# Kernel optimization log

Measured on AMD Instinct MI355X. Metric: run time of the kernel, lower is better.

The kernel has to match this reference:

```python
import jax, jax.numpy as jnp
import numpy as np

B, S, H = 2, 2048, 2048
NH, NKV, D = 16, 4, 128      # heads, kv heads, head_dim
GROUPS = NH // NKV
WIN = 1024                    # sliding window
EPS = 1e-5
THETA = 10000.0
NEG = -1e9


def _rms_norm(x, w):
    # over last dim (head_dim)
    var = jnp.mean(x * x, axis=-1, keepdims=True)
    return x * jax.lax.rsqrt(var + EPS) * w


def _rotate_half(x):
    x1, x2 = jnp.split(x, 2, axis=-1)
    return jnp.concatenate([-x2, x1], axis=-1)


def _apply_rope(q, k, cos, sin):
    # q: [B,NH,S,D], k: [B,NKV,S,D], cos/sin: [B,S,D]
    c = cos[:, None, :, :]
    s = sin[:, None, :, :]
    q = q * c + _rotate_half(q) * s
    k = k * c + _rotate_half(k) * s
    return q, k


def setup_inputs() -> dict:
    key = jax.random.key(0)
    ks = jax.random.split(key, 8)
    std = 0.02
    hidden_states = jax.random.normal(ks[0], (B, S, H), dtype=jnp.float32)
    Wq = jax.random.normal(ks[1], (NH * D, H), dtype=jnp.float32) * std
    Wk = jax.random.normal(ks[2], (NKV * D, H), dtype=jnp.float32) * std
    Wv = jax.random.normal(ks[3], (NKV * D, H), dtype=jnp.float32) * std
    Wo = jax.random.normal(ks[4], (H, NH * D), dtype=jnp.float32) * std
    Wg = jax.random.normal(ks[5], (NH * D, H), dtype=jnp.float32) * std
    q_norm_w = jnp.ones((D,), dtype=jnp.float32)
    k_norm_w = jnp.ones((D,), dtype=jnp.float32)
    # RoPE tables
    inv_freq = 1.0 / (THETA ** (jnp.arange(0, D, 2, dtype=jnp.float32) / D))
    pos = jnp.arange(S, dtype=jnp.float32)
    freqs = jnp.einsum('s,d->sd', pos, inv_freq)          # [S, D/2]
    emb = jnp.concatenate([freqs, freqs], axis=-1)        # [S, D]
    cos = jnp.broadcast_to(jnp.cos(emb)[None], (B, S, D)).astype(jnp.float32)
    sin = jnp.broadcast_to(jnp.sin(emb)[None], (B, S, D)).astype(jnp.float32)
    i = jnp.arange(S)[:, None]
    j = jnp.arange(S)[None, :]
    allowed = (j <= i) & (i - j < WIN)
    attention_mask = jnp.where(allowed, 0.0, NEG).astype(jnp.float32)[None, None]  # [1,1,S,S]
    return {
        'hidden_states': hidden_states, 'cos': cos, 'sin': sin,
        'attention_mask': attention_mask,
        'Wq': Wq, 'Wk': Wk, 'Wv': Wv, 'Wo': Wo, 'Wg': Wg,
        'q_norm_w': q_norm_w, 'k_norm_w': k_norm_w,
    }


def reference(hidden_states, cos, sin, attention_mask, Wq, Wk, Wv, Wo, Wg, q_norm_w, k_norm_w):
    x = hidden_states                                  # [B,S,H]
    q = (x @ Wq.T).reshape(B, S, NH, D)
    k = (x @ Wk.T).reshape(B, S, NKV, D)
    v = (x @ Wv.T).reshape(B, S, NKV, D)
    gate = x @ Wg.T                                    # [B,S,NH*D]
    q = _rms_norm(q, q_norm_w)
    k = _rms_norm(k, k_norm_w)
    q = q.transpose(0, 2, 1, 3)                        # [B,NH,S,D]
    k = k.transpose(0, 2, 1, 3)                        # [B,NKV,S,D]
    v = v.transpose(0, 2, 1, 3)
    # local (sliding) attention layer -> RoPE applied
    q, k = _apply_rope(q, k, cos, sin)
    # GQA: repeat kv heads
    k = jnp.repeat(k, GROUPS, axis=1)                  # [B,NH,S,D]
    v = jnp.repeat(v, GROUPS, axis=1)
    scaling = D ** -0.5
    scores = jnp.einsum('bhqd,bhkd->bhqk', q, k) * scaling
    scores = scores + attention_mask                   # broadcast [1,1,S,S]
    probs = jax.nn.softmax(scores.astype(jnp.float32), axis=-1).astype(q.dtype)
    out = jnp.einsum('bhqk,bhkd->bhqd', probs, v)      # [B,NH,S,D]
    out = out.transpose(0, 2, 1, 3).reshape(B, S, NH * D)
    out = out * jax.nn.sigmoid(gate)
    return out @ Wo.T                                  # [B,S,H]
```

## Files before the change

### kernel.cpp

```cpp
#include <hip/hip_runtime.h>
#include <hip/hip_bf16.h>

#define B_    2
#define S_    2048
#define H_    2048
#define NH_   16
#define NKV_  4
#define D_    128
#define WIN_  1024

typedef __attribute__((ext_vector_type(8))) short short8;
typedef __attribute__((ext_vector_type(4))) float f32x4;

__device__ __forceinline__ void gl2lds16(const void* g, void* l) {
  __builtin_amdgcn_global_load_lds(
      (const __attribute__((address_space(1))) void*)g,
      (__attribute__((address_space(3))) void*)l, 16, 0, 0);
}

__device__ __forceinline__ unsigned short f2bf(float x) {
  union { float f; unsigned int u; } v; v.f = x;
  unsigned int r = v.u + 0x7fffu + ((v.u >> 16) & 1u);
  return (unsigned short)(r >> 16);
}
__device__ __forceinline__ float bf2f(unsigned short u) {
  union { unsigned int i; float f; } v; v.i = ((unsigned int)u) << 16; return v.f;
}

#define CVT_TOTAL 5767168L
__global__ __launch_bounds__(256) void convert_all(
    const float* __restrict__ hs, const float* __restrict__ wq,
    const float* __restrict__ wk, const float* __restrict__ wv,
    const float* __restrict__ wg, const float* __restrict__ wo,
    unsigned short* __restrict__ xb, unsigned short* __restrict__ wall,
    unsigned short* __restrict__ wob) {
  long i = (long)blockIdx.x * 256 + threadIdx.x;
  if (i >= CVT_TOTAL) return;
  const float4* src; ushort4* dst;
  if (i < 2097152)      { src = (const float4*)hs + i;                         dst = (ushort4*)xb + i; }
  else if (i < 3145728) { long j = i - 2097152; src = (const float4*)wq + j;   dst = (ushort4*)wall + j; }
  else if (i < 3407872) { long j = i - 3145728; src = (const float4*)wk + j;   dst = (ushort4*)wall + 1048576 + j; }
  else if (i < 3670016) { long j = i - 3407872; src = (const float4*)wv + j;   dst = (ushort4*)wall + 1310720 + j; }
  else if (i < 4718592) { long j = i - 3670016; src = (const float4*)wg + j;   dst = (ushort4*)wall + 1572864 + j; }
  else                  { long j = i - 4718592; src = (const float4*)wo + j;   dst = (ushort4*)wob + j; }
  float4 v = *src;
  ushort4 o; o.x = f2bf(v.x); o.y = f2bf(v.y); o.z = f2bf(v.z); o.w = f2bf(v.w);
  *dst = o;
}

template <bool OUT_BF16>
__global__ __launch_bounds__(256) void gemm_bt(
    const unsigned short* __restrict__ A,
    const unsigned short* __restrict__ Bm,
    void* __restrict__ Cv, int M, int N, int K)
{
  __shared__ unsigned short As[128 * 64];
  __shared__ unsigned short Bs[128 * 64];
  const int t = threadIdx.x;
  const int lane = t & 63, wave = t >> 6;
  const int quad = lane >> 4, rl = lane & 15;
  const int bm = blockIdx.x * 128, bn = blockIdx.y * 128;
  const int wm = (wave >> 1) * 64, wn = (wave & 1) * 64;
  const int ldsbase = (t & ~63) * 8;

  f32x4 acc[4][4];
#pragma unroll
  for (int i = 0; i < 4; i++)
#pragma unroll
    for (int j = 0; j < 4; j++) acc[i][j] = (f32x4){0.f, 0.f, 0.f, 0.f};

  for (int k0 = 0; k0 < K; k0 += 64) {
#pragma unroll
    for (int i = 0; i < 4; i++) {
      int tt = i * 256 + t;
      int row = tt >> 3;
      int lc = (tt & 7) ^ (row & 7);
      gl2lds16(A + (long)(bm + row) * K + k0 + lc * 8, As + i * 2048 + ldsbase);
      gl2lds16(Bm + (long)(bn + row) * K + k0 + lc * 8, Bs + i * 2048 + ldsbase);
    }
    __syncthreads();
#pragma unroll
    for (int kk = 0; kk < 2; kk++) {
      short8 af[4], bfr[4];
#pragma unroll
      for (int i = 0; i < 4; i++) {
        int row = wm + i * 16 + rl;
        af[i] = *(const short8*)(As + row * 64 + (((kk * 4 + quad) ^ (row & 7)) * 8));
      }
#pragma unroll
      for (int j = 0; j < 4; j++) {
        int row = wn + j * 16 + rl;
        bfr[j] = *(const short8*)(Bs + row * 64 + (((kk * 4 + quad) ^ (row & 7)) * 8));
      }
#pragma unroll
      for (int i = 0; i < 4; i++)
#pragma unroll
        for (int j = 0; j < 4; j++)
          acc[i][j] = __builtin_amdgcn_mfma_f32_16x16x32_bf16(af[i], bfr[j], acc[i][j], 0, 0, 0);
    }
    __syncthreads();
  }
#pragma unroll
  for (int i = 0; i < 4; i++) {
    int row0 = bm + wm + i * 16 + quad * 4;
#pragma unroll
    for (int j = 0; j < 4; j++) {
      int col = bn + wn + j * 16 + rl;
#pragma unroll
      for (int r = 0; r < 4; r++) {
        if (OUT_BF16)
          ((unsigned short*)Cv)[(long)(row0 + r) * N + col] = f2bf(acc[i][j][r]);
        else
          ((float*)Cv)[(long)(row0 + r) * N + col] = acc[i][j][r];
      }
    }
  }
}

__global__ __launch_bounds__(256) void pack_and_transpose(
    const unsigned short* __restrict__ qkvg,
    const float* __restrict__ cosb, const float* __restrict__ sinb,
    const float* __restrict__ qw, const float* __restrict__ kw,
    unsigned short* __restrict__ qb, unsigned short* __restrict__ kb,
    unsigned short* __restrict__ vt)
{
  __shared__ unsigned short tile[64][136];
  int t = threadIdx.x;
  if (blockIdx.x >= 20480) {
    int blk = blockIdx.x - 20480;
    int st = blk & 31, kv = (blk >> 5) & 3, b = blk >> 7;
    int s0 = st * 64;
#pragma unroll
    for (int i = 0; i < 4; i++) {
      int idx = i * 256 + t;
      int r = idx >> 4, c = (idx & 15) * 8;
      short8 v = *(const short8*)(qkvg + (long)(b * S_ + s0 + r) * 5120 + 2560 + kv * 128 + c);
      *(short8*)(&tile[r][c]) = v;
    }
    __syncthreads();
    long vo = (long)(b * NKV_ + kv) * 128;
#pragma unroll
    for (int i = 0; i < 8; i++) {
      int idx = i * 256 + t;
      int d = idx >> 4, sc = idx & 15;
      ushort4 o;
      o.x = tile[sc * 4 + 0][d]; o.y = tile[sc * 4 + 1][d];
      o.z = tile[sc * 4 + 2][d]; o.w = tile[sc * 4 + 3][d];
      *(ushort4*)(vt + (vo + d) * S_ + s0 + sc * 4) = o;
    }
    return;
  }
  int lane = t & 63, wave = t >> 6;
  long gw = (long)blockIdx.x * 4 + wave;
  int hu = (int)(gw % 20);
  long bs = gw / 20;
  int b = (int)(bs / S_);
  int s = (int)(bs % S_);
  const unsigned short* row = qkvg + bs * 5120;

  bool isq = hu < 16;
  const unsigned short* base = isq ? (row + hu * 128) : (row + 2048 + (hu - 16) * 128);
  float x1 = bf2f(base[lane]), x2 = bf2f(base[lane + 64]);
  float ss = x1 * x1 + x2 * x2;
#pragma unroll
  for (int m = 1; m < 64; m <<= 1) ss += __shfl_xor(ss, m, 64);
  float inv = rsqrtf(ss * (1.0f / 128.0f) + 1e-5f);
  const float* w = isq ? qw : kw;
  float n1 = x1 * inv * w[lane], n2 = x2 * inv * w[lane + 64];
  const float* cp = cosb + bs * 128;
  const float* sp = sinb + bs * 128;
  float o1 = n1 * cp[lane] - n2 * sp[lane];
  float o2 = n2 * cp[lane + 64] + n1 * sp[lane + 64];
  if (isq) {
    long o = ((long)(b * NH_ + hu) * S_ + s) * 128;
    qb[o + lane] = f2bf(o1); qb[o + lane + 64] = f2bf(o2);
  } else {
    long o = ((long)(b * NKV_ + (hu - 16)) * S_ + s) * 128;
    kb[o + lane] = f2bf(o1); kb[o + lane + 64] = f2bf(o2);
  }
}

#define KSTR 136
#define VSTR 72
__global__ __launch_bounds__(256, 2) void attn_kernel(
    const unsigned short* __restrict__ qb,
    const unsigned short* __restrict__ kbuf,
    const unsigned short* __restrict__ vt,
    const unsigned short* __restrict__ qkvg,
    unsigned short* __restrict__ aout)
{
  __shared__ unsigned short Ks[64 * KSTR];
  __shared__ unsigned short Vs[128 * VSTR];
  __shared__ unsigned short Ps[4][2][16 * VSTR];
  int t = threadIdx.x, lane = t & 63, wave = t >> 6;
  int quad = lane >> 4, rl = lane & 15;
  int blk = blockIdx.x;
  int qh = blk & 1;
  int qt = 31 - ((blk >> 1) & 31);
  int kv = (blk >> 6) & 3, b = blk >> 8;
  int h = kv * 4 + wave;
  int q0 = qt * 64;

  const unsigned short* qhead = qb + (((long)(b * NH_ + h)) * S_) * 128;
  short8 qf[2][4];
#pragma unroll
  for (int mt = 0; mt < 2; mt++)
#pragma unroll
    for (int ks = 0; ks < 4; ks++)
      qf[mt][ks] = *(const short8*)(qhead +
          (long)(q0 + qh * 32 + mt * 16 + rl) * 128 + ks * 32 + quad * 8);

  f32x4 oacc[2][8];
#pragma unroll
  for (int mt = 0; mt < 2; mt++)
#pragma unroll
    for (int j = 0; j < 8; j++) oacc[mt][j] = (f32x4){0.f, 0.f, 0.f, 0.f};
  float m_r[2][4], l_r[2][4];
#pragma unroll
  for (int mt = 0; mt < 2; mt++)
#pragma unroll
    for (int r = 0; r < 4; r++) { m_r[mt][r] = -1e9f; l_r[mt][r] = 0.f; }

  const unsigned short* kbase_p = kbuf + ((long)(b * NKV_ + kv)) * S_ * 128;
  const unsigned short* vbase_p = vt + ((long)(b * NKV_ + kv)) * 128 * S_;
  int t_lo = qt - 16; if (t_lo < 0) t_lo = 0;

  int kr[4], kc[4], vr[4], vc[4];
#pragma unroll
  for (int i = 0; i < 4; i++) {
    int idx = i * 256 + t;
    kr[i] = idx >> 4; kc[i] = (idx & 15) * 8;
    vr[i] = idx >> 3; vc[i] = (idx & 7) * 8;
  }

  {
    int kb0 = t_lo * 64;
    short8 kv0[4], vv0[4];
#pragma unroll
    for (int i = 0; i < 4; i++) {
      kv0[i] = *(const short8*)(kbase_p + (long)(kb0 + kr[i]) * 128 + kc[i]);
      vv0[i] = *(const short8*)(vbase_p + (long)vr[i] * S_ + kb0 + vc[i]);
    }
#pragma unroll
    for (int i = 0; i < 4; i++) {
      *(short8*)(Ks + kr[i] * KSTR + kc[i]) = kv0[i];
      *(short8*)(Vs + vr[i] * VSTR + vc[i]) = vv0[i];
    }
  }
  __syncthreads();

  const float scale = 0.08838834764831845f;
  for (int kt = t_lo; kt <= qt; ++kt) {
    int kb0 = kt * 64;
    short8 kpre[4], vpre[4];
    if (kt < qt) {
      int nb0 = kb0 + 64;
#pragma unroll
      for (int i = 0; i < 4; i++) {
        kpre[i] = *(const short8*)(kbase_p + (long)(nb0 + kr[i]) * 128 + kc[i]);
        vpre[i] = *(const short8*)(vbase_p + (long)vr[i] * S_ + nb0 + vc[i]);
      }
    }

    f32x4 sc[2][4];
#pragma unroll
    for (int nt = 0; nt < 4; nt++) {
      f32x4 c0 = (f32x4){0.f, 0.f, 0.f, 0.f};
      f32x4 c1 = (f32x4){0.f, 0.f, 0.f, 0.f};
#pragma unroll
      for (int ks = 0; ks < 4; ks++) {
        short8 bfrag = *(const short8*)(Ks + (nt * 16 + rl) * KSTR + (ks * 4 + quad) * 8);
        c0 = __builtin_amdgcn_mfma_f32_16x16x32_bf16(qf[0][ks], bfrag, c0, 0, 0, 0);
        c1 = __builtin_amdgcn_mfma_f32_16x16x32_bf16(qf[1][ks], bfrag, c1, 0, 0, 0);
      }
      sc[0][nt] = c0; sc[1][nt] = c1;
    }
#pragma unroll
    for (int mt = 0; mt < 2; mt++) {
#pragma unroll
      for (int nt = 0; nt < 4; nt++)
#pragma unroll
        for (int r = 0; r < 4; r++) {
          int i_row = q0 + qh * 32 + mt * 16 + quad * 4 + r;
          int j_col = kb0 + nt * 16 + rl;
          bool ok = (j_col <= i_row) && (i_row - j_col < WIN_);
          sc[mt][nt][r] = ok ? sc[mt][nt][r] * scale : -1e9f;
        }
#pragma unroll
      for (int r = 0; r < 4; r++) {
        float mx = fmaxf(fmaxf(sc[mt][0][r], sc[mt][1][r]),
                         fmaxf(sc[mt][2][r], sc[mt][3][r]));
#pragma unroll
        for (int m = 1; m < 16; m <<= 1) mx = fmaxf(mx, __shfl_xor(mx, m, 64));
        float newm = fmaxf(m_r[mt][r], mx);
        float alpha = __expf(m_r[mt][r] - newm);
        float p0 = __expf(sc[mt][0][r] - newm), p1 = __expf(sc[mt][1][r] - newm);
        float p2 = __expf(sc[mt][2][r] - newm), p3 = __expf(sc[mt][3][r] - newm);
        float rs = p0 + p1 + p2 + p3;
#pragma unroll
        for (int m = 1; m < 16; m <<= 1) rs += __shfl_xor(rs, m, 64);
        l_r[mt][r] = l_r[mt][r] * alpha + rs;
        m_r[mt][r] = newm;
#pragma unroll
        for (int j = 0; j < 8; j++) oacc[mt][j][r] *= alpha;
        int prow = (quad * 4 + r) * VSTR;
        unsigned short* pw = &Ps[wave][mt][prow];
        pw[0 * 16 + rl] = f2bf(p0);
        pw[1 * 16 + rl] = f2bf(p1);
        pw[2 * 16 + rl] = f2bf(p2);
        pw[3 * 16 + rl] = f2bf(p3);
      }
    }
#pragma unroll
    for (int ks2 = 0; ks2 < 2; ks2++) {
      short8 af0 = *(const short8*)(&Ps[wave][0][rl * VSTR + (ks2 * 4 + quad) * 8]);
      short8 af1 = *(const short8*)(&Ps[wave][1][rl * VSTR + (ks2 * 4 + quad) * 8]);
#pragma unroll
      for (int j = 0; j < 8; j++) {
        short8 bf2 = *(const short8*)(Vs + (j * 16 + rl) * VSTR + (ks2 * 4 + quad) * 8);
        oacc[0][j] = __builtin_amdgcn_mfma_f32_16x16x32_bf16(af0, bf2, oacc[0][j], 0, 0, 0);
        oacc[1][j] = __builtin_amdgcn_mfma_f32_16x16x32_bf16(af1, bf2, oacc[1][j], 0, 0, 0);
      }
    }
    if (kt < qt) {
      __syncthreads();
#pragma unroll
      for (int i = 0; i < 4; i++) {
        *(short8*)(Ks + kr[i] * KSTR + kc[i]) = kpre[i];
        *(short8*)(Vs + vr[i] * VSTR + vc[i]) = vpre[i];
      }
      __syncthreads();
    }
  }

#pragma unroll
  for (int mt = 0; mt < 2; mt++)
#pragma unroll
    for (int r = 0; r < 4; r++) {
      int s_idx = q0 + qh * 32 + mt * 16 + quad * 4 + r;
      float invl = 1.0f / l_r[mt][r];
      long rowoff = (long)(b * S_ + s_idx);
      const unsigned short* grow = qkvg + rowoff * 5120 + 3072 + h * 128;
      unsigned short* orow = aout + rowoff * 2048 + h * 128;
#pragma unroll
      for (int j = 0; j < 8; j++) {
        int d = j * 16 + rl;
        float o = oacc[mt][j][r] * invl;
        float g = bf2f(grow[d]);
        o = o / (1.0f + __expf(-g));
        orow[d] = f2bf(o);
      }
    }
}

extern "C" void kernel_launch(void* const* d_in, const int* in_sizes, int n_in,
                              void* d_out, int out_size, void* d_ws, size_t ws_size,
                              hipStream_t stream) {
  (void)in_sizes; (void)n_in; (void)out_size; (void)ws_size;
  const float* hs   = (const float*)d_in[0];
  const float* cosb = (const float*)d_in[1];
  const float* sinb = (const float*)d_in[2];
  const float* Wq = (const float*)d_in[4];
  const float* Wk = (const float*)d_in[5];
  const float* Wv = (const float*)d_in[6];
  const float* Wo = (const float*)d_in[7];
  const float* Wg = (const float*)d_in[8];
  const float* qw = (const float*)d_in[9];
  const float* kw = (const float*)d_in[10];
  float* out = (float*)d_out;

  char* ws = (char*)d_ws;
  unsigned short* Xb   = (unsigned short*)ws; ws += (size_t)4096 * 2048 * 2;
  unsigned short* Wall = (unsigned short*)ws; ws += (size_t)5120 * 2048 * 2;
  unsigned short* Wob  = (unsigned short*)ws; ws += (size_t)2048 * 2048 * 2;
  unsigned short* qkvg = (unsigned short*)ws; ws += (size_t)4096 * 5120 * 2;
  unsigned short* qb   = (unsigned short*)ws; ws += (size_t)B_ * NH_ * S_ * D_ * 2;
  unsigned short* kbuf = (unsigned short*)ws; ws += (size_t)B_ * NKV_ * S_ * D_ * 2;
  unsigned short* vtb  = (unsigned short*)ws; ws += (size_t)B_ * NKV_ * S_ * D_ * 2;
  unsigned short* aout = (unsigned short*)ws; ws += (size_t)4096 * 2048 * 2;

  convert_all<<<(int)((CVT_TOTAL + 255) / 256), 256, 0, stream>>>(
      hs, Wq, Wk, Wv, Wg, Wo, Xb, Wall, Wob);
  gemm_bt<true><<<dim3(32, 40), 256, 0, stream>>>(Xb, Wall, (void*)qkvg, 4096, 5120, 2048);
  pack_and_transpose<<<20736, 256, 0, stream>>>(qkvg, cosb, sinb, qw, kw, qb, kbuf, vtb);
  attn_kernel<<<512, 256, 0, stream>>>(qb, kbuf, vtb, qkvg, aout);
  gemm_bt<false><<<dim3(32, 16), 256, 0, stream>>>(aout, Wob, (void*)out, 4096, 2048, 2048);
}
```

Baseline: 403.8 us.

## Split attention query tiles to 16 rows per wave, doubling grid and occupancy

Each wave now handles 16 query rows instead of 32, so the attention grid grows from 512 to 1024 blocks and launch bounds allow 3 blocks per CU. Block index decoding is reordered so blocks sharing a query tile sit next to each other, and the online-softmax rescale is skipped when no row max increases. MFMA sections are wrapped in s_setprio. The intent is more parallelism and less register pressure. The cost is that each K/V tile loaded into LDS is reused across fewer query rows, which adds global-to-LDS traffic.

After: 393.4 us. -2.6%, faster.

```diff
diff --git a/kernel.cpp b/kernel.cpp
--- a/kernel.cpp
+++ b/kernel.cpp
@@ -182,7 +182,8 @@
 
 #define KSTR 136
 #define VSTR 72
-__global__ __launch_bounds__(256, 2) void attn_kernel(
+#define PSTR 68
+__global__ __launch_bounds__(256, 3) void attn_kernel(
     const unsigned short* __restrict__ qb,
     const unsigned short* __restrict__ kbuf,
     const unsigned short* __restrict__ vt,
@@ -191,35 +192,29 @@
 {
   __shared__ unsigned short Ks[64 * KSTR];
   __shared__ unsigned short Vs[128 * VSTR];
-  __shared__ unsigned short Ps[4][2][16 * VSTR];
+  __shared__ unsigned short Ps[4][16 * PSTR];
   int t = threadIdx.x, lane = t & 63, wave = t >> 6;
   int quad = lane >> 4, rl = lane & 15;
   int blk = blockIdx.x;
-  int qh = blk & 1;
-  int qt = 31 - ((blk >> 1) & 31);
-  int kv = (blk >> 6) & 3, b = blk >> 8;
+  int qt = 31 - (blk >> 5);
+  int qu = blk & 3;
+  int kv = (blk >> 2) & 3;
+  int b  = (blk >> 4) & 1;
   int h = kv * 4 + wave;
-  int q0 = qt * 64;
+  int q0 = qt * 64 + qu * 16;
 
   const unsigned short* qhead = qb + (((long)(b * NH_ + h)) * S_) * 128;
-  short8 qf[2][4];
-#pragma unroll
-  for (int mt = 0; mt < 2; mt++)
-#pragma unroll
-    for (int ks = 0; ks < 4; ks++)
-      qf[mt][ks] = *(const short8*)(qhead +
-          (long)(q0 + qh * 32 + mt * 16 + rl) * 128 + ks * 32 + quad * 8);
-
-  f32x4 oacc[2][8];
-#pragma unroll
-  for (int mt = 0; mt < 2; mt++)
-#pragma unroll
-    for (int j = 0; j < 8; j++) oacc[mt][j] = (f32x4){0.f, 0.f, 0.f, 0.f};
-  float m_r[2][4], l_r[2][4];
-#pragma unroll
-  for (int mt = 0; mt < 2; mt++)
-#pragma unroll
-    for (int r = 0; r < 4; r++) { m_r[mt][r] = -1e9f; l_r[mt][r] = 0.f; }
+  short8 qf[4];
+#pragma unroll
+  for (int ks = 0; ks < 4; ks++)
+    qf[ks] = *(const short8*)(qhead + (long)(q0 + rl) * 128 + ks * 32 + quad * 8);
+
+  f32x4 oacc[8];
+#pragma unroll
+  for (int j = 0; j < 8; j++) oacc[j] = (f32x4){0.f, 0.f, 0.f, 0.f};
+  float m_r[4], l_r[4];
+#pragma unroll
+  for (int r = 0; r < 4; r++) { m_r[r] = -1e9f; l_r[r] = 0.f; }
 
   const unsigned short* kbase_p = kbuf + ((long)(b * NKV_ + kv)) * S_ * 128;
   const unsigned short* vbase_p = vt + ((long)(b * NKV_ + kv)) * 128 * S_;
@@ -262,66 +257,78 @@
       }
     }
 
-    f32x4 sc[2][4];
+    f32x4 sc[4];
+    __builtin_amdgcn_s_setprio(1);
 #pragma unroll
     for (int nt = 0; nt < 4; nt++) {
       f32x4 c0 = (f32x4){0.f, 0.f, 0.f, 0.f};
-      f32x4 c1 = (f32x4){0.f, 0.f, 0.f, 0.f};
 #pragma unroll
       for (int ks = 0; ks < 4; ks++) {
         short8 bfrag = *(const short8*)(Ks + (nt * 16 + rl) * KSTR + (ks * 4 + quad) * 8);
-        c0 = __builtin_amdgcn_mfma_f32_16x16x32_bf16(qf[0][ks], bfrag, c0, 0, 0, 0);
-        c1 = __builtin_amdgcn_mfma_f32_16x16x32_bf16(qf[1][ks], bfrag, c1, 0, 0, 0);
-      }
-      sc[0][nt] = c0; sc[1][nt] = c1;
-    }
-#pragma unroll
-    for (int mt = 0; mt < 2; mt++) {
-#pragma unroll
-      for (int nt = 0; nt < 4; nt++)
-#pragma unroll
-        for (int r = 0; r < 4; r++) {
-          int i_row = q0 + qh * 32 + mt * 16 + quad * 4 + r;
-          int j_col = kb0 + nt * 16 + rl;
-          bool ok = (j_col <= i_row) && (i_row - j_col < WIN_);
-          sc[mt][nt][r] = ok ? sc[mt][nt][r] * scale : -1e9f;
-        }
+        c0 = __builtin_amdgcn_mfma_f32_16x16x32_bf16(qf[ks], bfrag, c0, 0, 0, 0);
+      }
+      sc[nt] = c0;
+    }
+    __builtin_amdgcn_s_setprio(0);
+
+#pragma unroll
+    for (int nt = 0; nt < 4; nt++)
 #pragma unroll
       for (int r = 0; r < 4; r++) {
-        float mx = fmaxf(fmaxf(sc[mt][0][r], sc[mt][1][r]),
-                         fmaxf(sc[mt][2][r], sc[mt][3][r]));
-#pragma unroll
-        for (int m = 1; m < 16; m <<= 1) mx = fmaxf(mx, __shfl_xor(mx, m, 64));
-        float newm = fmaxf(m_r[mt][r], mx);
-        float alpha = __expf(m_r[mt][r] - newm);
-        float p0 = __expf(sc[mt][0][r] - newm), p1 = __expf(sc[mt][1][r] - newm);
-        float p2 = __expf(sc[mt][2][r] - newm), p3 = __expf(sc[mt][3][r] - newm);
-        float rs = p0 + p1 + p2 + p3;
-#pragma unroll
-        for (int m = 1; m < 16; m <<= 1) rs += __shfl_xor(rs, m, 64);
-        l_r[mt][r] = l_r[mt][r] * alpha + rs;
-        m_r[mt][r] = newm;
-#pragma unroll
-        for (int j = 0; j < 8; j++) oacc[mt][j][r] *= alpha;
-        int prow = (quad * 4 + r) * VSTR;
-        unsigned short* pw = &Ps[wave][mt][prow];
-        pw[0 * 16 + rl] = f2bf(p0);
-        pw[1 * 16 + rl] = f2bf(p1);
-        pw[2 * 16 + rl] = f2bf(p2);
-        pw[3 * 16 + rl] = f2bf(p3);
-      }
-    }
+        int i_row = q0 + quad * 4 + r;
+        int j_col = kb0 + nt * 16 + rl;
+        bool ok = (j_col <= i_row) && (i_row - j_col < WIN_);
+        sc[nt][r] = ok ? sc[nt][r] * scale : -1e9f;
+      }
+
+    float mx[4];
+#pragma unroll
+    for (int r = 0; r < 4; r++) {
+      float m0 = fmaxf(fmaxf(sc[0][r], sc[1][r]), fmaxf(sc[2][r], sc[3][r]));
+#pragma unroll
+      for (int m = 1; m < 16; m <<= 1) m0 = fmaxf(m0, __shfl_xor(m0, m, 64));
+      mx[r] = m0;
+    }
+    bool need = (mx[0] > m_r[0]) | (mx[1] > m_r[1]) |
+                (mx[2] > m_r[2]) | (mx[3] > m_r[3]);
+    if (__any(need)) {
+#pragma unroll
+      for (int r = 0; r < 4; r++) {
+        float newm = fmaxf(m_r[r], mx[r]);
+        float alpha = __expf(m_r[r] - newm);
+        l_r[r] *= alpha;
+#pragma unroll
+        for (int j = 0; j < 8; j++) oacc[j][r] *= alpha;
+        m_r[r] = newm;
+      }
+    }
+#pragma unroll
+    for (int r = 0; r < 4; r++) {
+      float p0 = __expf(sc[0][r] - m_r[r]), p1 = __expf(sc[1][r] - m_r[r]);
+      float p2 = __expf(sc[2][r] - m_r[r]), p3 = __expf(sc[3][r] - m_r[r]);
+      float rs = p0 + p1 + p2 + p3;
+#pragma unroll
+      for (int m = 1; m < 16; m <<= 1) rs += __shfl_xor(rs, m, 64);
+      l_r[r] += rs;
+      unsigned short* pw = &Ps[wave][(quad * 4 + r) * PSTR];
+      pw[0 * 16 + rl] = f2bf(p0);
+      pw[1 * 16 + rl] = f2bf(p1);
+      pw[2 * 16 + rl] = f2bf(p2);
+      pw[3 * 16 + rl] = f2bf(p3);
+    }
+
+    __builtin_amdgcn_s_setprio(1);
 #pragma unroll
     for (int ks2 = 0; ks2 < 2; ks2++) {
-      short8 af0 = *(const short8*)(&Ps[wave][0][rl * VSTR + (ks2 * 4 + quad) * 8]);
-      short8 af1 = *(const short8*)(&Ps[wave][1][rl * VSTR + (ks2 * 4 + quad) * 8]);
+      short8 af = *(const short8*)(&Ps[wave][rl * PSTR + (ks2 * 4 + quad) * 8]);
 #pragma unroll
       for (int j = 0; j < 8; j++) {
         short8 bf2 = *(const short8*)(Vs + (j * 16 + rl) * VSTR + (ks2 * 4 + quad) * 8);
-        oacc[0][j] = __builtin_amdgcn_mfma_f32_16x16x32_bf16(af0, bf2, oacc[0][j], 0, 0, 0);
-        oacc[1][j] = __builtin_amdgcn_mfma_f32_16x16x32_bf16(af1, bf2, oacc[1][j], 0, 0, 0);
-      }
-    }
+        oacc[j] = __builtin_amdgcn_mfma_f32_16x16x32_bf16(af, bf2, oacc[j], 0, 0, 0);
+      }
+    }
+    __builtin_amdgcn_s_setprio(0);
+
     if (kt < qt) {
       __syncthreads();
 #pragma unroll
@@ -334,23 +341,21 @@
   }
 
 #pragma unroll
-  for (int mt = 0; mt < 2; mt++)
-#pragma unroll
-    for (int r = 0; r < 4; r++) {
-      int s_idx = q0 + qh * 32 + mt * 16 + quad * 4 + r;
-      float invl = 1.0f / l_r[mt][r];
-      long rowoff = (long)(b * S_ + s_idx);
-      const unsigned short* grow = qkvg + rowoff * 5120 + 3072 + h * 128;
-      unsigned short* orow = aout + rowoff * 2048 + h * 128;
-#pragma unroll
-      for (int j = 0; j < 8; j++) {
-        int d = j * 16 + rl;
-        float o = oacc[mt][j][r] * invl;
-        float g = bf2f(grow[d]);
-        o = o / (1.0f + __expf(-g));
-        orow[d] = f2bf(o);
-      }
-    }
+  for (int r = 0; r < 4; r++) {
+    int s_idx = q0 + quad * 4 + r;
+    float invl = 1.0f / l_r[r];
+    long rowoff = (long)(b * S_ + s_idx);
+    const unsigned short* gptr = qkvg + rowoff * 5120 + 3072 + h * 128;
+    unsigned short* orow = aout + rowoff * 2048 + h * 128;
+#pragma unroll
+    for (int j = 0; j < 8; j++) {
+      int d = j * 16 + rl;
+      float o = oacc[j][r] * invl;
+      float g = bf2f(gptr[d]);
+      o = o / (1.0f + __expf(-g));
+      orow[d] = f2bf(o);
+    }
+  }
 }
 
 extern "C" void kernel_launch(void* const* d_in, const int* in_sizes, int n_in,
@@ -383,6 +388,6 @@
       hs, Wq, Wk, Wv, Wg, Wo, Xb, Wall, Wob);
   gemm_bt<true><<<dim3(32, 40), 256, 0, stream>>>(Xb, Wall, (void*)qkvg, 4096, 5120, 2048);
   pack_and_transpose<<<20736, 256, 0, stream>>>(qkvg, cosb, sinb, qw, kw, qb, kbuf, vtb);
-  attn_kernel<<<512, 256, 0, stream>>>(qb, kbuf, vtb, qkvg, aout);
+  attn_kernel<<<1024, 256, 0, stream>>>(qb, kbuf, vtb, qkvg, aout);
   gemm_bt<false><<<dim3(32, 16), 256, 0, stream>>>(aout, Wob, (void*)out, 4096, 2048, 2048);
 }
```
